# Optimization experiments

Measured on AMD Instinct MI355X. Metric: run time of the kernel, lower is better.

The kernel has to match this reference:

```python
import jax, jax.numpy as jnp
import numpy as np

BS = 4096
D = 256
TAU = 0.5
EPS = 1e-08          # eps added to negative-sum denominator (module arg)
COS_EPS = 1e-08      # nn.CosineSimilarity norm clamp


def setup_inputs() -> dict:
    key = jax.random.key(0)
    k1, k2 = jax.random.split(key)
    zi = jax.random.normal(k1, (BS, D), dtype=jnp.float32)
    zj = jax.random.normal(k2, (BS, D), dtype=jnp.float32)
    return {"zi": zi, "zj": zj}


def reference(zi, zj):
    bs = zi.shape[0]
    n = 2 * bs
    z = jnp.concatenate([zi, zj], axis=0)                       # [2bs, D]
    # cosine similarity = normalized dot products (norms clamped like torch)
    norm = jnp.linalg.norm(z, axis=-1, keepdims=True)
    zn = z / jnp.maximum(norm, COS_EPS)
    sim = jnp.matmul(zn, zn.T) / TAU                            # [2bs, 2bs]
    e = jnp.exp(sim)
    # positive pairs: row i pairs with column (i+bs) mod 2bs
    rows = jnp.arange(n)
    pair = jnp.concatenate([jnp.arange(bs) + bs, jnp.arange(bs)])
    sim_pos = e[rows, pair]                                     # [2bs]
    # negatives: all entries in a row except the diagonal
    sim_neg_sum = e.sum(axis=-1) - jnp.diagonal(e)              # [2bs]
    loss = jnp.mean(-jnp.log(sim_pos / (sim_neg_sum + EPS)))
    return loss
```

## Files before the change

kernel.cpp:

```cpp
#include <hip/hip_runtime.h>
#include <hip/hip_bf16.h>


#define N_ROWS 8192
#define BSZ    4096
#define DIM    256
#define INV_TAU 2.0f
#define EPS_REF 1e-8f
#define COS_EPS 1e-8f
#define NG2     64
#define NTILES  (NG2 * (NG2 + 1) / 2)
#define LSTRIDE 260

typedef __attribute__((ext_vector_type(4))) float f32x4;
typedef long long i64;
typedef union { int4 v; i64 d[2]; } pack16;

__device__ __forceinline__ float red16(float x) {
    x += __int_as_float(__builtin_amdgcn_update_dpp(0, __float_as_int(x), 0x121, 0xf, 0xf, false));
    x += __int_as_float(__builtin_amdgcn_update_dpp(0, __float_as_int(x), 0x122, 0xf, 0xf, false));
    x += __int_as_float(__builtin_amdgcn_update_dpp(0, __float_as_int(x), 0x124, 0xf, 0xf, false));
    x += __int_as_float(__builtin_amdgcn_update_dpp(0, __float_as_int(x), 0x128, 0xf, 0xf, false));
    return x;
}

__global__ __launch_bounds__(256) void knorm(const float* __restrict__ zi,
                                             const float* __restrict__ zj,
                                             unsigned char* __restrict__ znsw,
                                             float* __restrict__ out) {
    __shared__ float lds[16 * LSTRIDE];
    __shared__ float nrm[16];
    const int rg = blockIdx.x;
    const int t  = threadIdx.x;
    const int w  = t >> 6;
    const int l  = t & 63;
    const int row0 = rg * 16;
    if (rg == 0 && t == 0) out[0] = 0.f;

    #pragma unroll
    for (int s = 0; s < 4; ++s) {
        const int row = s * 4 + w;
        const int r   = row0 + row;
        const float* src = (r < BSZ) ? zi + (size_t)r * DIM + l * 4
                                     : zj + (size_t)(r - BSZ) * DIM + l * 4;
        const float4 v = *(const float4*)src;
        *(float4*)&lds[row * LSTRIDE + l * 4] = v;
        float ss = v.x*v.x + v.y*v.y + v.z*v.z + v.w*v.w;
        #pragma unroll
        for (int off = 32; off >= 1; off >>= 1) ss += __shfl_xor(ss, off);
        if (l == 0) nrm[row] = 1.0f / fmaxf(sqrtf(ss), COS_EPS);
    }
    __syncthreads();

    const int kbp = w, fl = l;
    const int r16 = fl & 15, q = fl >> 4;
    const float inv = nrm[r16];
    int wd[4];
    #pragma unroll
    for (int h = 0; h < 2; ++h) {
        const int kk = (2 * kbp + h) * 32 + q * 8;
        float f[8];
        #pragma unroll
        for (int j = 0; j < 8; ++j) f[j] = lds[r16 * LSTRIDE + kk + j] * inv;
        int a = 0, b = 0;
        a = __builtin_amdgcn_cvt_pk_fp8_f32(f[0], f[1], a, false);
        a = __builtin_amdgcn_cvt_pk_fp8_f32(f[2], f[3], a, true);
        b = __builtin_amdgcn_cvt_pk_fp8_f32(f[4], f[5], b, false);
        b = __builtin_amdgcn_cvt_pk_fp8_f32(f[6], f[7], b, true);
        wd[h * 2] = a; wd[h * 2 + 1] = b;
    }
    *(int4*)(znsw + ((size_t)(rg * 4 + kbp) * 64 + fl) * 16) =
        make_int4(wd[0], wd[1], wd[2], wd[3]);
}

__global__ __launch_bounds__(256, 4) void kgemm(const unsigned char* __restrict__ znsw,
                                                float* __restrict__ P,
                                                float* __restrict__ selfdot,
                                                float* __restrict__ pairdot) {
    __shared__ __align__(16) unsigned char pan[32768];
    const int w = threadIdx.x >> 6;
    const int l = threadIdx.x & 63;

    const int t = blockIdx.x;
    int Gi = (int)((129.0f - sqrtf(16641.0f - 8.0f * (float)t)) * 0.5f);
    while ((Gi + 1) * (129 - (Gi + 1)) / 2 <= t) ++Gi;
    while (Gi * (129 - Gi) / 2 > t) --Gi;
    const int Gj = Gi + (t - Gi * (129 - Gi) / 2);

    const char* srcA = (const char*)znsw + (size_t)Gi * 32768;
    #pragma unroll
    for (int sub = 0; sub < 8; ++sub) {
        const int off = sub * 4096 + w * 1024;
        __builtin_amdgcn_global_load_lds(
            (const __attribute__((address_space(1))) void*)(srcA + off + l * 16),
            (__attribute__((address_space(3))) void*)(&pan[off]), 16, 0, 0);
    }

    const int rh = w >> 1, ch = w & 1;
    const char* Ap    = (const char*)&pan[0] + rh * 16384 + l * 16;
    const char* bbase = (const char*)znsw + (size_t)Gj * 32768 + ch * 16384 + l * 16;

    pack16 Bcur[4], Bnxt[4];
    #pragma unroll
    for (int nt = 0; nt < 4; ++nt)
        Bcur[nt].v = *(const int4*)(bbase + nt * 4096);

    f32x4 acc[4][4];
    #pragma unroll
    for (int mt = 0; mt < 4; ++mt)
        #pragma unroll
        for (int nt = 0; nt < 4; ++nt)
            acc[mt][nt] = (f32x4){0.f, 0.f, 0.f, 0.f};

    __syncthreads();

    #pragma unroll
    for (int kbp = 0; kbp < 4; ++kbp) {
        if (kbp < 3) {
            #pragma unroll
            for (int nt = 0; nt < 4; ++nt)
                Bnxt[nt].v = *(const int4*)(bbase + nt * 4096 + (kbp + 1) * 1024);
        }
        pack16 Afr[4];
        #pragma unroll
        for (int mt = 0; mt < 4; ++mt)
            Afr[mt].v = *(const int4*)(Ap + mt * 4096 + kbp * 1024);
        #pragma unroll
        for (int mt = 0; mt < 4; ++mt)
            #pragma unroll
            for (int nt = 0; nt < 4; ++nt) {
                acc[mt][nt] = __builtin_amdgcn_mfma_f32_16x16x32_fp8_fp8(
                    Afr[mt].d[0], Bcur[nt].d[0], acc[mt][nt], 0, 0, 0);
                acc[mt][nt] = __builtin_amdgcn_mfma_f32_16x16x32_fp8_fp8(
                    Afr[mt].d[1], Bcur[nt].d[1], acc[mt][nt], 0, 0, 0);
            }
        #pragma unroll
        for (int nt = 0; nt < 4; ++nt) Bcur[nt] = Bnxt[nt];
    }

    const int c = l & 15, q = l >> 4;
    const int rsel = c - 4 * q;
    const bool vld = (rsel >= 0) && (rsel < 4);

    if ((Gi == Gj || Gj == Gi + 32) && rh == ch) {
        float dv[4];
        #pragma unroll
        for (int mt = 0; mt < 4; ++mt) {
            float d = acc[mt][mt][0];
            #pragma unroll
            for (int r = 1; r < 4; ++r)
                if (rsel == r) d = acc[mt][mt][r];
            dv[mt] = d;
        }
        if (vld) {
            float* dst = (Gi == Gj) ? selfdot : pairdot;
            #pragma unroll
            for (int mt = 0; mt < 4; ++mt)
                dst[Gi * 128 + rh * 64 + mt * 16 + c] = dv[mt];
        }
    }

    #pragma unroll
    for (int mt = 0; mt < 4; ++mt)
        #pragma unroll
        for (int nt = 0; nt < 4; ++nt)
            #pragma unroll
            for (int r = 0; r < 4; ++r)
                acc[mt][nt][r] = __expf(acc[mt][nt][r] * INV_TAU);

    float rs[4][4];
    #pragma unroll
    for (int mt = 0; mt < 4; ++mt)
        #pragma unroll
        for (int r = 0; r < 4; ++r)
            rs[mt][r] = red16(acc[mt][0][r] + acc[mt][1][r] + acc[mt][2][r] + acc[mt][3][r]);
    if (c == 0) {
        #pragma unroll
        for (int mt = 0; mt < 4; ++mt) {
            const f32x4 o4 = (f32x4){rs[mt][0], rs[mt][1], rs[mt][2], rs[mt][3]};
            __builtin_nontemporal_store(o4,
                (f32x4*)&P[(size_t)(Gj * 2 + ch) * N_ROWS + Gi * 128 + rh * 64 + mt * 16 + q * 4]);
        }
    }

    if (Gi != Gj) {
        float cs[4];
        #pragma unroll
        for (int nt = 0; nt < 4; ++nt) {
            float s = 0.f;
            #pragma unroll
            for (int mt = 0; mt < 4; ++mt)
                #pragma unroll
                for (int r = 0; r < 4; ++r)
                    s += acc[mt][nt][r];
            s += __shfl_xor(s, 16);
            s += __shfl_xor(s, 32);
            cs[nt] = s;
        }
        if (q == 0) {
            #pragma unroll
            for (int nt = 0; nt < 4; ++nt)
                __builtin_nontemporal_store(cs[nt],
                    &P[(size_t)(Gi * 2 + rh) * N_ROWS + Gj * 128 + ch * 64 + nt * 16 + c]);
        }
    }
}

__global__ __launch_bounds__(256) void kfinal(const float* __restrict__ P,
                                              const float* __restrict__ selfdot,
                                              const float* __restrict__ pairdot,
                                              float* __restrict__ out) {
    const int l = threadIdx.x & 63;
    const int w = threadIdx.x >> 6;
    const int row = blockIdx.x * 64 + l;
    float s = 0.f;
    #pragma unroll
    for (int st = 0; st < 32; ++st)
        s += P[(size_t)(w * 32 + st) * N_ROWS + row];
    __shared__ float wsum[4][64];
    wsum[w][l] = s;
    __syncthreads();
    if (w == 0) {
        const float tot = wsum[0][l] + wsum[1][l] + wsum[2][l] + wsum[3][l];
        const float selfe = __expf(selfdot[row] * INV_TAU);
        const float pd    = pairdot[(row < BSZ) ? row : row - BSZ];
        float loss = logf(tot - selfe + EPS_REF) - pd * INV_TAU;
        #pragma unroll
        for (int off = 32; off >= 1; off >>= 1) loss += __shfl_xor(loss, off);
        if (l == 0) atomicAdd(out, loss * (1.0f / (float)N_ROWS));
    }
}

extern "C" void kernel_launch(void* const* d_in, const int* in_sizes, int n_in,
                              void* d_out, int out_size, void* d_ws, size_t ws_size,
                              hipStream_t stream) {
    const float* zi = (const float*)d_in[0];
    const float* zj = (const float*)d_in[1];
    float* out = (float*)d_out;

    char* ws = (char*)d_ws;
    unsigned char* znsw = (unsigned char*)ws;
    float* P       = (float*)(ws + 2 * 1024 * 1024);
    float* selfdot = (float*)(ws + 6 * 1024 * 1024);
    float* pairdot = (float*)(ws + 6 * 1024 * 1024 + 32 * 1024);

    knorm <<<N_ROWS / 16, 256, 0, stream>>>(zi, zj, znsw, out);
    kgemm <<<NTILES, 256, 0, stream>>>(znsw, P, selfdot, pairdot);
    kfinal<<<N_ROWS / 64, 256, 0, stream>>>(P, selfdot, pairdot, out);
}
```

Baseline: 86.20 us.

## Switch fp8 GEMM to 16x16x128 scaled MFMA with K-major fragment layout

The GEMM now uses the gfx950 scaled MFMA 16x16x128 f8f6f4 instruction with unit scales instead of pairs of 16x16x32 fp8 MFMAs, cutting the MFMA instruction count by a factor of four. The normalize kernel repacks the fp8 output so each lane holds 32 contiguous K bytes per 128-K block, matching the new operand layout. B fragments are loaded in two halves rather than a four-step rolling prefetch, and the occupancy hint drops from 4 to 2 blocks per CU to allow more registers. The risks are layout mismatches between producer and consumer, and lower occupancy hiding less memory latency.

Result: faster. 82.94 us (-3.8%).

```diff
diff --git a/kernel.cpp b/kernel.cpp
--- a/kernel.cpp
+++ b/kernel.cpp
@@ -13,8 +13,8 @@
 #define LSTRIDE 260
 
 typedef __attribute__((ext_vector_type(4))) float f32x4;
-typedef long long i64;
-typedef union { int4 v; i64 d[2]; } pack16;
+typedef __attribute__((ext_vector_type(8))) int   v8i;
+typedef union { int4 x[2]; v8i v; } frag32;
 
 __device__ __forceinline__ float red16(float x) {
     x += __int_as_float(__builtin_amdgcn_update_dpp(0, __float_as_int(x), 0x121, 0xf, 0xf, false));
@@ -52,28 +52,27 @@
     }
     __syncthreads();
 
-    const int kbp = w, fl = l;
+    const int pi = t >> 6, fl = t & 63;
+    const int h = pi >> 1, p = pi & 1;
     const int r16 = fl & 15, q = fl >> 4;
+    const int k0 = h * 128 + q * 32 + p * 16;
     const float inv = nrm[r16];
+    float f[16];
+    #pragma unroll
+    for (int j = 0; j < 16; ++j) f[j] = lds[r16 * LSTRIDE + k0 + j] * inv;
     int wd[4];
     #pragma unroll
-    for (int h = 0; h < 2; ++h) {
-        const int kk = (2 * kbp + h) * 32 + q * 8;
-        float f[8];
-        #pragma unroll
-        for (int j = 0; j < 8; ++j) f[j] = lds[r16 * LSTRIDE + kk + j] * inv;
-        int a = 0, b = 0;
-        a = __builtin_amdgcn_cvt_pk_fp8_f32(f[0], f[1], a, false);
-        a = __builtin_amdgcn_cvt_pk_fp8_f32(f[2], f[3], a, true);
-        b = __builtin_amdgcn_cvt_pk_fp8_f32(f[4], f[5], b, false);
-        b = __builtin_amdgcn_cvt_pk_fp8_f32(f[6], f[7], b, true);
-        wd[h * 2] = a; wd[h * 2 + 1] = b;
-    }
-    *(int4*)(znsw + ((size_t)(rg * 4 + kbp) * 64 + fl) * 16) =
+    for (int g = 0; g < 4; ++g) {
+        int a = 0;
+        a = __builtin_amdgcn_cvt_pk_fp8_f32(f[g*4+0], f[g*4+1], a, false);
+        a = __builtin_amdgcn_cvt_pk_fp8_f32(f[g*4+2], f[g*4+3], a, true);
+        wd[g] = a;
+    }
+    *(int4*)(znsw + (size_t)rg * 4096 + pi * 1024 + fl * 16) =
         make_int4(wd[0], wd[1], wd[2], wd[3]);
 }
 
-__global__ __launch_bounds__(256, 4) void kgemm(const unsigned char* __restrict__ znsw,
+__global__ __launch_bounds__(256, 2) void kgemm(const unsigned char* __restrict__ znsw,
                                                 float* __restrict__ P,
                                                 float* __restrict__ selfdot,
                                                 float* __restrict__ pairdot) {
@@ -97,13 +96,14 @@
     }
 
     const int rh = w >> 1, ch = w & 1;
-    const char* Ap    = (const char*)&pan[0] + rh * 16384 + l * 16;
-    const char* bbase = (const char*)znsw + (size_t)Gj * 32768 + ch * 16384 + l * 16;
-
-    pack16 Bcur[4], Bnxt[4];
-    #pragma unroll
-    for (int nt = 0; nt < 4; ++nt)
-        Bcur[nt].v = *(const int4*)(bbase + nt * 4096);
+    const char* bbase = (const char*)znsw + (size_t)Gj * 32768 + ch * 4 * 4096 + l * 16;
+
+    frag32 B0[4], B1[4];
+    #pragma unroll
+    for (int nt = 0; nt < 4; ++nt) {
+        B0[nt].x[0] = *(const int4*)(bbase + nt * 4096);
+        B0[nt].x[1] = *(const int4*)(bbase + nt * 4096 + 1024);
+    }
 
     f32x4 acc[4][4];
     #pragma unroll
@@ -115,27 +115,32 @@
     __syncthreads();
 
     #pragma unroll
-    for (int kbp = 0; kbp < 4; ++kbp) {
-        if (kbp < 3) {
-            #pragma unroll
-            for (int nt = 0; nt < 4; ++nt)
-                Bnxt[nt].v = *(const int4*)(bbase + nt * 4096 + (kbp + 1) * 1024);
-        }
-        pack16 Afr[4];
+    for (int h = 0; h < 2; ++h) {
+        if (h == 0) {
+            #pragma unroll
+            for (int nt = 0; nt < 4; ++nt) {
+                B1[nt].x[0] = *(const int4*)(bbase + nt * 4096 + 2048);
+                B1[nt].x[1] = *(const int4*)(bbase + nt * 4096 + 3072);
+            }
+        }
+        frag32 A[4];
+        #pragma unroll
+        for (int mt = 0; mt < 4; ++mt) {
+            const char* ap = (const char*)&pan[(rh * 4 + mt) * 4096 + h * 2048] + l * 16;
+            A[mt].x[0] = *(const int4*)(ap);
+            A[mt].x[1] = *(const int4*)(ap + 1024);
+        }
         #pragma unroll
         for (int mt = 0; mt < 4; ++mt)
-            Afr[mt].v = *(const int4*)(Ap + mt * 4096 + kbp * 1024);
-        #pragma unroll
-        for (int mt = 0; mt < 4; ++mt)
             #pragma unroll
             for (int nt = 0; nt < 4; ++nt) {
-                acc[mt][nt] = __builtin_amdgcn_mfma_f32_16x16x32_fp8_fp8(
-                    Afr[mt].d[0], Bcur[nt].d[0], acc[mt][nt], 0, 0, 0);
-                acc[mt][nt] = __builtin_amdgcn_mfma_f32_16x16x32_fp8_fp8(
-                    Afr[mt].d[1], Bcur[nt].d[1], acc[mt][nt], 0, 0, 0);
+                const v8i bv = (h == 0) ? B0[nt].v : B1[nt].v;
+                acc[mt][nt] = __builtin_amdgcn_mfma_scale_f32_16x16x128_f8f6f4(
+                    A[mt].v, bv, acc[mt][nt],
+                    0, 0,
+                    0, 0x7f7f7f7f,
+                    0, 0x7f7f7f7f);
             }
-        #pragma unroll
-        for (int nt = 0; nt < 4; ++nt) Bcur[nt] = Bnxt[nt];
     }
 
     const int c = l & 15, q = l >> 4;
```
